# Kernel optimization log

Measured on AMD Instinct MI355X. Metric: run time of the kernel, lower is better.

The kernel has to match this reference:

```python
import jax, jax.numpy as jnp
import numpy as np

B, T, C = 512, 256, 192
HEAD = 64

def setup_inputs() -> dict:
    key = jax.random.key(0)
    ks = jax.random.split(key, 5)
    return {
        "x": jax.random.normal(ks[0], (B, T, C), dtype=jnp.float32),
        "Wk": jax.random.normal(ks[1], (C, HEAD), dtype=jnp.float32) * (C ** -0.5),
        "Wq": jax.random.normal(ks[2], (C, HEAD), dtype=jnp.float32) * (C ** -0.5),
        "Wv": jax.random.normal(ks[3], (C, HEAD), dtype=jnp.float32) * (C ** -0.5),
        "pos_table": jax.random.normal(ks[4], (T, C), dtype=jnp.float32),
    }

def reference(x, Wk, Wq, Wv, pos_table):
    Bx, Tx, Cx = x.shape
    scale = Cx ** -0.5  # note: scales by n_embed, not head_size (faithful to source)
    k = jnp.einsum('btc,ch->bth', x, Wk)
    q = jnp.einsum('btc,ch->bth', x, Wq)
    v = jnp.einsum('btc,ch->bth', x, Wv)
    pe = pos_table[:Tx]                       # [T, C]
    pos_k = pe @ Wk                           # [T, H]
    pos_q = pe @ Wq                           # [T, H]
    bias = pos_k @ pos_q.T                    # [T, T]
    wei = jnp.einsum('bqh,bkh->bqk', q, k) * scale + bias
    causal = jnp.tril(jnp.ones((Tx, Tx), dtype=bool))
    wei = jnp.where(causal, wei, -jnp.inf)
    wei = jax.nn.softmax(wei, axis=-1)
    # dropout is identity in inference mode
    out = jnp.einsum('bqk,bkh->bqh', wei, v)
    return out
```

## Files before the change

kernel.cpp:

```cpp
#include <hip/hip_runtime.h>
#include <hip/hip_bf16.h>

typedef unsigned short u16;
typedef unsigned int u32;
using bf16x8 = __attribute__((ext_vector_type(8))) short;
using f32x4  = __attribute__((ext_vector_type(4))) float;

#define BB 512
#define TT 256
#define CC 192
#define HH 64

__device__ __forceinline__ u16 f2bf(float f) {
    __hip_bfloat16 h = __float2bfloat16(f);
    u16 u; __builtin_memcpy(&u, &h, 2); return u;
}


__global__ void wprep_kernel(const float* __restrict__ Wq,
                             const float* __restrict__ Wk,
                             const float* __restrict__ Wv,
                             u16* __restrict__ W_sw) {
    int gid  = blockIdx.x * 256 + threadIdx.x;
    int fid  = gid >> 6, lane = gid & 63;
    int n3   = fid / 6,  ks   = fid % 6;
    int l15  = lane & 15, quad = lane >> 4;
    const float* W = (n3 < 4) ? Wq : (n3 < 8) ? Wk : Wv;
    const int h = (n3 & 3) * 16 + l15;
    u16* dst = W_sw + (size_t)gid * 8;
    #pragma unroll
    for (int u = 0; u < 8; ++u) {
        int c = ks * 32 + quad * 8 + u;
        dst[u] = f2bf(W[c * HH + h]);
    }
}

__global__ void pos_kernel(const float* __restrict__ Wk,
                           const float* __restrict__ Wq,
                           const float* __restrict__ pe,
                           float* __restrict__ poskT, float* __restrict__ posqT) {
    int t = blockIdx.x * 4 + (threadIdx.x >> 6);
    int h = threadIdx.x & 63;
    float ak = 0.f, aq = 0.f;
    for (int c = 0; c < CC; ++c) {
        float p = pe[t * CC + c];
        ak += p * Wk[c * HH + h];
        aq += p * Wq[c * HH + h];
    }
    poskT[h * TT + t] = ak;
    posqT[h * TT + t] = aq;
}

__global__ void bias_kernel(const float* __restrict__ poskT,
                            const float* __restrict__ posqT,
                            float4* __restrict__ bias_sw) {
    const int i = blockIdx.x >> 4, jt = blockIdx.x & 15;
    if (jt > i) return;
    const int lane = threadIdx.x;
    const int l15 = lane & 15, quad = lane >> 4;
    const int tq = i * 16 + quad * 4;
    const int jc = jt * 16 + l15;
    float s[4] = {0.f, 0.f, 0.f, 0.f};
    for (int h = 0; h < HH; ++h) {
        float pq = posqT[h * TT + jc];
        #pragma unroll
        for (int r = 0; r < 4; ++r)
            s[r] += poskT[h * TT + tq + r] * pq;
    }
    bias_sw[blockIdx.x * 64 + lane] = make_float4(s[0], s[1], s[2], s[3]);
}

#define XP 200

__global__ __launch_bounds__(256, 4)
void qkv_kernel(const float* __restrict__ x,
                const u16* __restrict__ W_sw,
                u16* __restrict__ q_sw, u16* __restrict__ k_sw,
                u16* __restrict__ vg) {
    __shared__ __align__(16) u16 xs[64 * XP];
    const int tid  = threadIdx.x;
    const int w    = tid >> 6;
    const int lane = tid & 63;
    const int l15  = lane & 15;
    const int quad = lane >> 4;
    const int b    = blockIdx.x >> 2;
    const int rb   = blockIdx.x & 3;
    const float* xb = x + ((size_t)b * TT + rb * 64) * CC;

    #pragma unroll
    for (int it = 0; it < 12; ++it) {
        const int flat = (it * 256 + tid) * 4;
        const int row = flat / CC, col = flat % CC;
        const float4 v = *(const float4*)(xb + flat);
        uint2 pk;
        pk.x = (u32)f2bf(v.x) | ((u32)f2bf(v.y) << 16);
        pk.y = (u32)f2bf(v.z) | ((u32)f2bf(v.w) << 16);
        *(uint2*)&xs[row * XP + col] = pk;
    }
    __syncthreads();

    const bf16x8* Wv8 = (const bf16x8*)W_sw;
    f32x4 acc[12];
    #pragma unroll
    for (int n = 0; n < 12; ++n) acc[n] = {0.f, 0.f, 0.f, 0.f};
    #pragma unroll
    for (int ks = 0; ks < 6; ++ks) {
        const bf16x8 a = *(const bf16x8*)&xs[(w * 16 + l15) * XP + ks * 32 + quad * 8];
        #pragma unroll
        for (int n = 0; n < 12; ++n)
            acc[n] = __builtin_amdgcn_mfma_f32_16x16x32_bf16(a, Wv8[(n * 6 + ks) * 64 + lane], acc[n], 0, 0, 0);
    }

    const int i_loc  = rb * 4 + w;
    const size_t bi  = (size_t)b * 16 + i_loc;
    const int u   = l15 & 7;
    #pragma unroll
    for (int n = 0; n < 4; ++n) {
        const int hs    = n >> 1;
        const int quadp = (n * 2 + (l15 >> 3)) & 3;
        const size_t base = (bi * 2 + hs) * 512 + (quadp * 16 + quad * 4) * 8 + u;
        #pragma unroll
        for (int r = 0; r < 4; ++r) {
            q_sw[base + r * 8] = f2bf(acc[n][r]);
            k_sw[base + r * 8] = f2bf(acc[4 + n][r]);
        }
    }
    const size_t t_glob = (size_t)b * TT + i_loc * 16;
    #pragma unroll
    for (int n = 0; n < 4; ++n)
    #pragma unroll
    for (int r = 0; r < 4; ++r)
        vg[(t_glob + quad * 4 + r) * HH + n * 16 + l15] = f2bf(acc[8 + n][r]);
}

#define VP 264
#define PP 40
#define VT_ELEMS (HH * VP)
#define P_ELEMS 640
#define LDSB_ELEMS (VT_ELEMS + 4 * P_ELEMS)

__global__ __launch_bounds__(256, 4)
void attn_kernel(const u16* __restrict__ q_sw, const u16* __restrict__ k_sw,
                 const u16* __restrict__ vg, const float4* __restrict__ bias_sw,
                 float* __restrict__ out) {
    __shared__ __align__(16) u16 lds[LDSB_ELEMS];
    const int tid  = threadIdx.x;
    const int w    = tid >> 6;
    const int lane = tid & 63;
    const int l15  = lane & 15;
    const int quad = lane >> 4;
    const int b    = blockIdx.x >> 1;
    const int half = blockIdx.x & 1;

    {
        const u16* vrow = vg + ((size_t)b * TT + tid) * HH;
        #pragma unroll
        for (int u2 = 0; u2 < 8; ++u2) {
            bf16x8 vv = *(const bf16x8*)(vrow + u2 * 8);
            #pragma unroll
            for (int e = 0; e < 8; ++e)
                lds[(u2 * 8 + e) * VP + tid] = (u16)vv[e];
        }
    }
    __syncthreads();

    u16* Pw = &lds[VT_ELEMS + w * P_ELEMS];
    const float scale = 0.07216878364870322f;
    const f32x4 zero4 = {0.f, 0.f, 0.f, 0.f};
    const bf16x8* qv = (const bf16x8*)q_sw;
    const bf16x8* kv = (const bf16x8*)k_sw;

    #pragma unroll 1
    for (int mt = 0; mt < 2; ++mt) {
        const int i  = half ? (mt ? 11 - w : 4 + w) : (mt ? 15 - w : w);
        const int t0 = 16 * i;
        const int J  = i + 1;
        const int Pq = (J + 1) >> 1;
        const size_t bi = (size_t)b * 16 + i;

        const bf16x8 qf0 = qv[(bi * 2 + 0) * 64 + lane];
        const bf16x8 qf1 = qv[(bi * 2 + 1) * 64 + lane];

        f32x4 o[4];
        float m4[4], l4[4];
        #pragma unroll
        for (int n = 0; n < 4; ++n) o[n] = zero4;
        #pragma unroll
        for (int r = 0; r < 4; ++r) { m4[r] = -1e30f; l4[r] = 0.f; }

        #pragma unroll
        for (int p = 0; p < 8; ++p) {
            if (p < Pq) {
                const int jt0 = 2 * p, jt1 = 2 * p + 1;
                f32x4 sa = zero4, sb;
                {
                    const size_t bj = (size_t)b * 16 + jt0;
                    bf16x8 k0 = kv[(bj * 2 + 0) * 64 + lane];
                    bf16x8 k1 = kv[(bj * 2 + 1) * 64 + lane];
                    sa = __builtin_amdgcn_mfma_f32_16x16x32_bf16(qf0, k0, sa, 0, 0, 0);
                    sa = __builtin_amdgcn_mfma_f32_16x16x32_bf16(qf1, k1, sa, 0, 0, 0);
                    const float4 b4 = bias_sw[(i * 16 + jt0) * 64 + lane];
                    sa[0] = sa[0] * scale + b4.x;
                    sa[1] = sa[1] * scale + b4.y;
                    sa[2] = sa[2] * scale + b4.z;
                    sa[3] = sa[3] * scale + b4.w;
                    if (jt0 == i) {
                        #pragma unroll
                        for (int r = 0; r < 4; ++r)
                            if (l15 > quad * 4 + r) sa[r] = -1e30f;
                    }
                }
                if (jt1 < J) {
                    sb = zero4;
                    const size_t bj = (size_t)b * 16 + jt1;
                    bf16x8 k0 = kv[(bj * 2 + 0) * 64 + lane];
                    bf16x8 k1 = kv[(bj * 2 + 1) * 64 + lane];
                    sb = __builtin_amdgcn_mfma_f32_16x16x32_bf16(qf0, k0, sb, 0, 0, 0);
                    sb = __builtin_amdgcn_mfma_f32_16x16x32_bf16(qf1, k1, sb, 0, 0, 0);
                    const float4 b4 = bias_sw[(i * 16 + jt1) * 64 + lane];
                    sb[0] = sb[0] * scale + b4.x;
                    sb[1] = sb[1] * scale + b4.y;
                    sb[2] = sb[2] * scale + b4.z;
                    sb[3] = sb[3] * scale + b4.w;
                    if (jt1 == i) {
                        #pragma unroll
                        for (int r = 0; r < 4; ++r)
                            if (l15 > quad * 4 + r) sb[r] = -1e30f;
                    }
                } else {
                    sb[0] = -1e30f; sb[1] = -1e30f; sb[2] = -1e30f; sb[3] = -1e30f;
                }
                float t4[4];
                #pragma unroll
                for (int r = 0; r < 4; ++r) t4[r] = fmaxf(sa[r], sb[r]);
                #pragma unroll
                for (int d = 1; d < 16; d <<= 1) {
                    #pragma unroll
                    for (int r = 0; r < 4; ++r) t4[r] = fmaxf(t4[r], __shfl_xor(t4[r], d, 64));
                }
                float al[4];
                #pragma unroll
                for (int r = 0; r < 4; ++r) {
                    float mn = fmaxf(m4[r], t4[r]);
                    al[r] = __expf(m4[r] - mn);
                    m4[r] = mn;
                    l4[r] *= al[r];
                }
                #pragma unroll
                for (int n = 0; n < 4; ++n)
                #pragma unroll
                for (int r = 0; r < 4; ++r) o[n][r] *= al[r];
                #pragma unroll
                for (int r = 0; r < 4; ++r) {
                    float e0 = __expf(sa[r] - m4[r]);
                    float e1 = __expf(sb[r] - m4[r]);
                    l4[r] += e0 + e1;
                    Pw[(quad * 4 + r) * PP + l15]      = f2bf(e0);
                    Pw[(quad * 4 + r) * PP + 16 + l15] = f2bf(e1);
                }
                bf16x8 pa = *(const bf16x8*)&Pw[l15 * PP + quad * 8];
                #pragma unroll
                for (int n = 0; n < 4; ++n) {
                    bf16x8 bv = *(const bf16x8*)&lds[(n * 16 + l15) * VP + p * 32 + quad * 8];
                    o[n] = __builtin_amdgcn_mfma_f32_16x16x32_bf16(pa, bv, o[n], 0, 0, 0);
                }
            }
        }
        #pragma unroll
        for (int d = 1; d < 16; d <<= 1) {
            #pragma unroll
            for (int r = 0; r < 4; ++r) l4[r] += __shfl_xor(l4[r], d, 64);
        }
        float rl4[4];
        #pragma unroll
        for (int r = 0; r < 4; ++r) rl4[r] = 1.f / l4[r];
        float* ob = out + ((size_t)b * TT + t0) * HH;
        #pragma unroll
        for (int n = 0; n < 4; ++n)
        #pragma unroll
        for (int r = 0; r < 4; ++r)
            ob[(quad * 4 + r) * HH + n * 16 + l15] = o[n][r] * rl4[r];
    }
}

extern "C" void kernel_launch(void* const* d_in, const int* in_sizes, int n_in,
                              void* d_out, int out_size, void* d_ws, size_t ws_size,
                              hipStream_t stream) {
    const float* x  = (const float*)d_in[0];
    const float* Wk = (const float*)d_in[1];
    const float* Wq = (const float*)d_in[2];
    const float* Wv = (const float*)d_in[3];
    const float* pe = (const float*)d_in[4];
    float* out = (float*)d_out;

    float*  poskT  = (float*)d_ws;
    float*  posqT  = poskT + TT * HH;
    float4* biassw = (float4*)(posqT + TT * HH);
    u16*    W_sw   = (u16*)((float*)biassw + TT * TT);
    u16*    q_sw   = W_sw + 3 * HH * CC;
    u16*    k_sw   = q_sw + (size_t)BB * TT * HH;
    u16*    vg     = k_sw + (size_t)BB * TT * HH;

    wprep_kernel<<<18, 256, 0, stream>>>(Wq, Wk, Wv, W_sw);
    pos_kernel<<<TT / 4, 256, 0, stream>>>(Wk, Wq, pe, poskT, posqT);
    bias_kernel<<<256, 64, 0, stream>>>(poskT, posqT, biassw);
    qkv_kernel<<<4 * BB, 256, 0, stream>>>(x, W_sw, q_sw, k_sw, vg);
    attn_kernel<<<2 * BB, 256, 0, stream>>>(q_sw, k_sw, vg, biassw, out);
}
```

Baseline: 240.5 us.

## Repartition QKV projection so each wave owns output columns and caches weights

The QKV projection kernel's work split changes. Each wave now covers all 64 rows of the tile and one 16-column slice of each of Q, K and V, instead of 16 rows and all 192 output columns. The wave's 18 weight fragments are loaded into registers before the x staging, so the global weight reads overlap the LDS fill and are not repeated inside the MFMA loop. The costs are four LDS A-fragment reads per k-step instead of one, higher register pressure, and launch bounds lowered from 4 to 3 blocks per SM to make room.

```diff
diff --git a/kernel.cpp b/kernel.cpp
--- a/kernel.cpp
+++ b/kernel.cpp
@@ -72,7 +72,7 @@
 
 #define XP 200
 
-__global__ __launch_bounds__(256, 4)
+__global__ __launch_bounds__(256, 3)
 void qkv_kernel(const float* __restrict__ x,
                 const u16* __restrict__ W_sw,
                 u16* __restrict__ q_sw, u16* __restrict__ k_sw,
@@ -87,6 +87,14 @@
     const int rb   = blockIdx.x & 3;
     const float* xb = x + ((size_t)b * TT + rb * 64) * CC;
 
+    const bf16x8* Wv8 = (const bf16x8*)W_sw;
+    bf16x8 Wf[18];
+    #pragma unroll
+    for (int mat = 0; mat < 3; ++mat)
+        #pragma unroll
+        for (int ks = 0; ks < 6; ++ks)
+            Wf[mat * 6 + ks] = Wv8[(((mat * 4 + w) * 6) + ks) * 64 + lane];
+
     #pragma unroll
     for (int it = 0; it < 12; ++it) {
         const int flat = (it * 256 + tid) * 4;
@@ -99,38 +107,41 @@
     }
     __syncthreads();
 
-    const bf16x8* Wv8 = (const bf16x8*)W_sw;
     f32x4 acc[12];
     #pragma unroll
-    for (int n = 0; n < 12; ++n) acc[n] = {0.f, 0.f, 0.f, 0.f};
+    for (int i = 0; i < 12; ++i) acc[i] = {0.f, 0.f, 0.f, 0.f};
     #pragma unroll
     for (int ks = 0; ks < 6; ++ks) {
-        const bf16x8 a = *(const bf16x8*)&xs[(w * 16 + l15) * XP + ks * 32 + quad * 8];
-        #pragma unroll
-        for (int n = 0; n < 12; ++n)
-            acc[n] = __builtin_amdgcn_mfma_f32_16x16x32_bf16(a, Wv8[(n * 6 + ks) * 64 + lane], acc[n], 0, 0, 0);
-    }
-
-    const int i_loc  = rb * 4 + w;
-    const size_t bi  = (size_t)b * 16 + i_loc;
-    const int u   = l15 & 7;
-    #pragma unroll
-    for (int n = 0; n < 4; ++n) {
-        const int hs    = n >> 1;
-        const int quadp = (n * 2 + (l15 >> 3)) & 3;
+        bf16x8 a[4];
+        #pragma unroll
+        for (int m = 0; m < 4; ++m)
+            a[m] = *(const bf16x8*)&xs[(m * 16 + l15) * XP + ks * 32 + quad * 8];
+        #pragma unroll
+        for (int m = 0; m < 4; ++m)
+            #pragma unroll
+            for (int mat = 0; mat < 3; ++mat)
+                acc[m * 3 + mat] = __builtin_amdgcn_mfma_f32_16x16x32_bf16(
+                    a[m], Wf[mat * 6 + ks], acc[m * 3 + mat], 0, 0, 0);
+    }
+
+    const int hs    = w >> 1;
+    const int quadp = (w * 2 + (l15 >> 3)) & 3;
+    const int u     = l15 & 7;
+    #pragma unroll
+    for (int m = 0; m < 4; ++m) {
+        const int i_loc  = rb * 4 + m;
+        const size_t bi  = (size_t)b * 16 + i_loc;
         const size_t base = (bi * 2 + hs) * 512 + (quadp * 16 + quad * 4) * 8 + u;
         #pragma unroll
         for (int r = 0; r < 4; ++r) {
-            q_sw[base + r * 8] = f2bf(acc[n][r]);
-            k_sw[base + r * 8] = f2bf(acc[4 + n][r]);
+            q_sw[base + r * 8] = f2bf(acc[m * 3 + 0][r]);
+            k_sw[base + r * 8] = f2bf(acc[m * 3 + 1][r]);
         }
-    }
-    const size_t t_glob = (size_t)b * TT + i_loc * 16;
-    #pragma unroll
-    for (int n = 0; n < 4; ++n)
-    #pragma unroll
-    for (int r = 0; r < 4; ++r)
-        vg[(t_glob + quad * 4 + r) * HH + n * 16 + l15] = f2bf(acc[8 + n][r]);
+        const size_t t_glob = (size_t)b * TT + i_loc * 16;
+        #pragma unroll
+        for (int r = 0; r < 4; ++r)
+            vg[(t_glob + quad * 4 + r) * HH + w * 16 + l15] = f2bf(acc[m * 3 + 2][r]);
+    }
 }
 
 #define VP 264
```

After: 219.2 us. 8.9% less time.
